# Performance work log

Hardware: AMD Instinct MI355X
Metric: run time of the kernel (lower is better)

## Reference

```python
import jax, jax.numpy as jnp
import numpy as np
from jax import lax

ALPHA = 0.5
GAMMA = 0.01
BIG = 1e8  # stands in for +inf boundary of the soft-DTW DP table


def _softmin3(a, b, c, gamma):
    x = jnp.stack([a, b, c], axis=0)
    return -gamma * jax.nn.logsumexp(-x / gamma, axis=0)


def _softdtw_values(D, gamma):
    """Soft-DTW values for a batch of cost matrices.

    D: [M, N, N] pairwise cost matrices -> [M] soft-DTW values R[N, N].
    Computed with an anti-diagonal lax.scan (2N-1 sequential steps), fully
    vectorized over the batch and over each diagonal.
    """
    M, N, _ = D.shape
    Dpad = jnp.zeros((M, N + 1, N + 1), D.dtype).at[:, 1:, 1:].set(D)
    ii = jnp.arange(N + 1)
    # diagonal d=0: only R[0,0]=0 ; diagonal d=1: R[0,1]=R[1,0]=inf
    prev2 = jnp.full((M, N + 1), BIG, D.dtype).at[:, 0].set(0.0)
    prev1 = jnp.full((M, N + 1), BIG, D.dtype)

    def shift(r):  # r at index i-1, BIG at i=0
        return jnp.concatenate([jnp.full((M, 1), BIG, r.dtype), r[:, :-1]], axis=1)

    def step(carry, d):
        p2, p1 = carry
        j = d - ii
        valid = (ii >= 1) & (ii <= N) & (j >= 1) & (j <= N)
        jc = jnp.clip(j, 0, N)
        dvals = Dpad[:, ii, jc]  # [M, N+1] costs on this diagonal
        # R[i,j] = D[i,j] + softmin(R[i-1,j-1], R[i-1,j], R[i,j-1])
        smin = _softmin3(shift(p2), shift(p1), p1, gamma)
        cur = jnp.where(valid[None, :], dvals + smin, BIG)
        return (p1, cur), None

    (_, cur), _ = lax.scan(step, (prev2, prev1), jnp.arange(2, 2 * N + 1))
    return cur[:, N]  # R[N, N]


def setup_inputs() -> dict:
    key = jax.random.key(0)
    k1, k2 = jax.random.split(key)
    outputs = jax.random.normal(k1, (64, 128, 4), dtype=jnp.float32)
    targets = jax.random.normal(k2, (64, 128, 4), dtype=jnp.float32)
    return {"outputs": outputs, "targets": targets}


def reference(outputs, targets):
    B, T, C = outputs.shape
    # Per (sample, channel): D[i, j] = (target_i - output_j)^2  (rows = target idx)
    t = jnp.transpose(targets, (0, 2, 1)).reshape(B * C, T)
    o = jnp.transpose(outputs, (0, 2, 1)).reshape(B * C, T)
    D = (t[:, :, None] - o[:, None, :]) ** 2  # [B*C, T, T]

    # shape loss: mean over batch of soft-DTW values, summed over channels
    vals = _softdtw_values(D, GAMMA)  # [B*C]
    loss_shape = vals.sum() / B

    # temporal loss: soft alignment path E = d(softDTW)/dD, penalized by (i-j)^2
    path = jax.grad(lambda DD: _softdtw_values(DD, GAMMA).sum())(D)  # [B*C, T, T]
    idx = jnp.arange(1, T + 1, dtype=D.dtype)
    Omega = (idx[:, None] - idx[None, :]) ** 2  # [T, T]
    loss_temporal = (path * Omega).sum() / (B * T * T)

    return ALPHA * loss_shape + (1.0 - ALPHA) * loss_temporal
```

## Files before the change

kernel.cpp:

```cpp
#include <hip/hip_runtime.h>


#define TN 128
#define BATCH 64
#define CH 4

__device__ __forceinline__ float fast_exp2(float x) { return __builtin_amdgcn_exp2f(x); }
__device__ __forceinline__ float fast_log2(float x) { return __builtin_amdgcn_logf(x); }
__device__ __forceinline__ float fast_rcp(float x)  { return __builtin_amdgcn_rcpf(x); }

__device__ __forceinline__ float dpp_shr1(float x, float fill) {
  union { float f; int i; } o, s, r;
  o.f = fill; s.f = x;
  r.i = __builtin_amdgcn_update_dpp(o.i, s.i, 0x138, 0xF, 0xF, false);
  return r.f;
}

__global__ __launch_bounds__(64)
void dilate_softdtw_kernel(const float* __restrict__ outputs,
                           const float* __restrict__ targets,
                           float* __restrict__ out) {
  __shared__ float obuf[384];

  const float WALLP = -4.328085e6f;
  const float O_PAD = 15.0f;
  const float K2    = 144.2695040888963f;

  const int m = blockIdx.x, b = m >> 2, c = m & 3;
  const int lane = threadIdx.x;
  const int i0 = 2*lane + 1;

  const float* tb = targets + (size_t)b*(TN*CH) + c;
  const float* ob = outputs + (size_t)b*(TN*CH) + c;

  #pragma unroll
  for (int s = 0; s < 6; ++s) {
    const int idx = lane + 64*s;
    const int k = idx - 126;
    obuf[idx] = ((unsigned)k <= 127u) ? ob[k*CH] : O_PAD;
  }
  const float t0 = tb[(i0 - 1)*CH];
  const float t1 = tb[i0*CH];
  __syncthreads();

  const float* oc = obuf + 126;

  float p1_0, p1_1 = WALLP, p2_0 = WALLP, up2 = WALLP;
  float dp1_0 = 0.f, dp1_1 = 0.f, dp2_0 = 0.f, dup2 = 0.f;
  {
    float df = t0 - oc[0];
    p1_0 = (lane == 0) ? -K2*df*df : WALLP;
  }
  float fd0 = (float)(2*i0 - 3);
  float fd1 = fd0 + 2.0f;
  float o0 = oc[2 - i0];
  float o1 = oc[1 - i0];

  #pragma unroll 4
  for (int d = 3; d <= 2*TN; ++d) {
    const int j0 = d - i0;
    const float o_nxt = oc[j0];
    float up1  = dpp_shr1(p1_1, WALLP);
    float dup1 = dpp_shr1(dp1_1, 0.f);

    float mn1 = fmaxf(p2_0, fmaxf(p1_0, p1_1));
    float mn0 = fmaxf(up2,  fmaxf(up1,  p1_0));
    float a1 = p2_0 - mn1, b1 = p1_0 - mn1, c1 = p1_1 - mn1;
    float a0 = up2  - mn0, b0 = up1  - mn0, c0 = p1_0 - mn0;

    float ea1 = fast_exp2(a1);
    float eb1 = fast_exp2(b1);
    float ec1 = fast_exp2(c1);
    float ea0 = fast_exp2(a0);
    float eb0 = fast_exp2(b0);
    float ec0 = fast_exp2(c0);

    float sum1 = (ea1 + eb1) + ec1;
    float sum0 = (ea0 + eb0) + ec0;
    float rs1 = fast_rcp(sum1);
    float rs0 = fast_rcp(sum0);
    float l1  = fast_log2(sum1);
    float l0  = fast_log2(sum0);

    float df1 = t1 - o1, df0 = t0 - o0;
    float q1 = df1*df1,  q0 = df0*df0;
    float jv1 = __builtin_fmaf(ea1, dp2_0, __builtin_fmaf(eb1, dp1_0, ec1*dp1_1));
    float jv0 = __builtin_fmaf(ea0, dup2,  __builtin_fmaf(eb0, dup1,  ec0*dp1_0));
    float w1 = fd1*fd1, w0 = fd0*fd0;

    float c1v = __builtin_fmaf(-K2, q1, mn1 + l1);
    float c0v = __builtin_fmaf(-K2, q0, mn0 + l0);
    float d1v = __builtin_fmaf(rs1, jv1, w1);
    float d0v = __builtin_fmaf(rs0, jv0, w0);

    p2_0 = p1_0;   p1_0 = c0v;  p1_1 = c1v;  up2 = up1;
    dp2_0 = dp1_0; dp1_0 = d0v; dp1_1 = d1v; dup2 = dup1;
    o1 = o0; o0 = o_nxt;
    fd0 -= 1.0f; fd1 -= 1.0f;
  }

  if (lane == 63) {
    const float partial = __builtin_fmaf(p1_1, -5.415212348e-5f,
                                         dp1_1 * 4.76837158203125e-7f);
    atomicAdd(out, partial);
  }
}

extern "C" void kernel_launch(void* const* d_in, const int* in_sizes, int n_in,
                              void* d_out, int out_size, void* d_ws, size_t ws_size,
                              hipStream_t stream) {
  const float* outputs = (const float*)d_in[0];
  const float* targets = (const float*)d_in[1];
  float* out = (float*)d_out;
  (void)in_sizes; (void)n_in; (void)out_size; (void)d_ws; (void)ws_size;

  (void)hipMemsetAsync(out, 0, sizeof(float), stream);
  dilate_softdtw_kernel<<<dim3(256), dim3(64), 0, stream>>>(outputs, targets, out);
}
```

Baseline: 84.23 us.

## Split soft-DTW rows into two one-row-per-lane wavefront phases via LDS boundary

Replaces the scheme where each lane owns two adjacent DP rows with two sequential phases. In each phase a lane owns a single row: rows 0-63 first, then rows 64-127. Lane 63 writes its row values and gradients to shared memory, and the second phase reads them as the DPP fill value for the row boundary. This halves the per-step arithmetic but raises the number of sequential anti-diagonal steps and removes the two-cell ILP per step, on a kernel that runs one wave per block and is likely latency-bound.

```diff
diff --git a/kernel.cpp b/kernel.cpp
--- a/kernel.cpp
+++ b/kernel.cpp
@@ -21,6 +21,7 @@
                            const float* __restrict__ targets,
                            float* __restrict__ out) {
   __shared__ float obuf[384];
+  __shared__ float2 Bb[192];
 
   const float WALLP = -4.328085e6f;
   const float O_PAD = 15.0f;
@@ -28,7 +29,6 @@
 
   const int m = blockIdx.x, b = m >> 2, c = m & 3;
   const int lane = threadIdx.x;
-  const int i0 = 2*lane + 1;
 
   const float* tb = targets + (size_t)b*(TN*CH) + c;
   const float* ob = outputs + (size_t)b*(TN*CH) + c;
@@ -39,69 +39,93 @@
     const int k = idx - 126;
     obuf[idx] = ((unsigned)k <= 127u) ? ob[k*CH] : O_PAD;
   }
-  const float t0 = tb[(i0 - 1)*CH];
-  const float t1 = tb[i0*CH];
+  const float tA = tb[lane*CH];
+  const float tB = tb[(64 + lane)*CH];
   __syncthreads();
 
   const float* oc = obuf + 126;
 
-  float p1_0, p1_1 = WALLP, p2_0 = WALLP, up2 = WALLP;
-  float dp1_0 = 0.f, dp1_1 = 0.f, dp2_0 = 0.f, dup2 = 0.f;
+  float rRes = 0.f, dRes = 0.f;
+
   {
-    float df = t0 - oc[0];
-    p1_0 = (lane == 0) ? -K2*df*df : WALLP;
+    const float t0 = tA;
+    float p1  = WALLP;
+    float up2 = (lane == 0) ? 0.0f : WALLP;
+    float dp1 = 0.f, dup2 = 0.f;
+    float fd  = (float)(2*lane);
+    float o0  = oc[-lane];
+
+    #pragma unroll 4
+    for (int d = 2; d <= 192; ++d) {
+      const int j0 = d - 1 - lane;
+      const float o_nxt = oc[j0];
+      float up1  = dpp_shr1(p1, WALLP);
+      float dup1 = dpp_shr1(dp1, 0.f);
+
+      float mn = fmaxf(up2, fmaxf(up1, p1));
+      float a = up2 - mn, bq = up1 - mn, cc = p1 - mn;
+      float ea = fast_exp2(a);
+      float eb = fast_exp2(bq);
+      float ec = fast_exp2(cc);
+      float sum = (ea + eb) + ec;
+      float rs = fast_rcp(sum);
+      float l  = fast_log2(sum);
+      float df = t0 - o0;
+      float q  = df*df;
+      float jv = __builtin_fmaf(ea, dup2, __builtin_fmaf(eb, dup1, ec*dp1));
+      float w  = fd*fd;
+      float cv = __builtin_fmaf(-K2, q, mn + l);
+      float dv = __builtin_fmaf(rs, jv, w);
+
+      if (lane == 63) Bb[d - 1] = make_float2(cv, dv);
+
+      up2 = up1; p1 = cv; dup2 = dup1; dp1 = dv;
+      o0 = o_nxt; fd -= 1.0f;
+    }
   }
-  float fd0 = (float)(2*i0 - 3);
-  float fd1 = fd0 + 2.0f;
-  float o0 = oc[2 - i0];
-  float o1 = oc[1 - i0];
+  __syncthreads();
 
-  #pragma unroll 4
-  for (int d = 3; d <= 2*TN; ++d) {
-    const int j0 = d - i0;
-    const float o_nxt = oc[j0];
-    float up1  = dpp_shr1(p1_1, WALLP);
-    float dup1 = dpp_shr1(dp1_1, 0.f);
+  {
+    const float t0 = tB;
+    float p1  = WALLP, up2 = WALLP;
+    float dp1 = 0.f, dup2 = 0.f;
+    float fd  = (float)(64 + 2*lane);
+    float o0  = oc[-lane];
+    float2 bc = Bb[64];
 
-    float mn1 = fmaxf(p2_0, fmaxf(p1_0, p1_1));
-    float mn0 = fmaxf(up2,  fmaxf(up1,  p1_0));
-    float a1 = p2_0 - mn1, b1 = p1_0 - mn1, c1 = p1_1 - mn1;
-    float a0 = up2  - mn0, b0 = up1  - mn0, c0 = p1_0 - mn0;
+    #pragma unroll 4
+    for (int d = 66; d <= 256; ++d) {
+      const int j0 = d - 65 - lane;
+      const float o_nxt = oc[j0];
+      const int bi = (d - 1 > 191) ? 191 : (d - 1);
+      const float2 bn = Bb[bi];
+      float up1  = dpp_shr1(p1, bc.x);
+      float dup1 = dpp_shr1(dp1, bc.y);
 
-    float ea1 = fast_exp2(a1);
-    float eb1 = fast_exp2(b1);
-    float ec1 = fast_exp2(c1);
-    float ea0 = fast_exp2(a0);
-    float eb0 = fast_exp2(b0);
-    float ec0 = fast_exp2(c0);
+      float mn = fmaxf(up2, fmaxf(up1, p1));
+      float a = up2 - mn, bq = up1 - mn, cc = p1 - mn;
+      float ea = fast_exp2(a);
+      float eb = fast_exp2(bq);
+      float ec = fast_exp2(cc);
+      float sum = (ea + eb) + ec;
+      float rs = fast_rcp(sum);
+      float l  = fast_log2(sum);
+      float df = t0 - o0;
+      float q  = df*df;
+      float jv = __builtin_fmaf(ea, dup2, __builtin_fmaf(eb, dup1, ec*dp1));
+      float w  = fd*fd;
+      float cv = __builtin_fmaf(-K2, q, mn + l);
+      float dv = __builtin_fmaf(rs, jv, w);
 
-    float sum1 = (ea1 + eb1) + ec1;
-    float sum0 = (ea0 + eb0) + ec0;
-    float rs1 = fast_rcp(sum1);
-    float rs0 = fast_rcp(sum0);
-    float l1  = fast_log2(sum1);
-    float l0  = fast_log2(sum0);
-
-    float df1 = t1 - o1, df0 = t0 - o0;
-    float q1 = df1*df1,  q0 = df0*df0;
-    float jv1 = __builtin_fmaf(ea1, dp2_0, __builtin_fmaf(eb1, dp1_0, ec1*dp1_1));
-    float jv0 = __builtin_fmaf(ea0, dup2,  __builtin_fmaf(eb0, dup1,  ec0*dp1_0));
-    float w1 = fd1*fd1, w0 = fd0*fd0;
-
-    float c1v = __builtin_fmaf(-K2, q1, mn1 + l1);
-    float c0v = __builtin_fmaf(-K2, q0, mn0 + l0);
-    float d1v = __builtin_fmaf(rs1, jv1, w1);
-    float d0v = __builtin_fmaf(rs0, jv0, w0);
-
-    p2_0 = p1_0;   p1_0 = c0v;  p1_1 = c1v;  up2 = up1;
-    dp2_0 = dp1_0; dp1_0 = d0v; dp1_1 = d1v; dup2 = dup1;
-    o1 = o0; o0 = o_nxt;
-    fd0 -= 1.0f; fd1 -= 1.0f;
+      up2 = up1; p1 = cv; dup2 = dup1; dp1 = dv;
+      o0 = o_nxt; fd -= 1.0f; bc = bn;
+    }
+    rRes = p1; dRes = dp1;
   }
 
   if (lane == 63) {
-    const float partial = __builtin_fmaf(p1_1, -5.415212348e-5f,
-                                         dp1_1 * 4.76837158203125e-7f);
+    const float partial = __builtin_fmaf(rRes, -5.415212348e-5f,
+                                         dRes * 4.76837158203125e-7f);
     atomicAdd(out, partial);
   }
 }
```

Measured after the change: 83.44 us. Within noise of the previous version (-0.9%).
